# Optimization experiments

Measured on AMD Instinct MI355X. Metric: run time of the kernel, lower is better.

## Reference

```python
import jax, jax.numpy as jnp
import numpy as np

D_MODEL, D_FFN, N_LEVELS, N_HEADS, N_POINTS = 256, 1024, 4, 8, 4
B, LQ = 2, 8192
SHAPES = [(128, 128), (64, 64), (32, 32), (16, 16)]  # (H_l, W_l) per level
D_HEAD = D_MODEL // N_HEADS


def setup_inputs() -> dict:
    key = jax.random.key(0)
    ks = jax.random.split(key, 16)
    S = sum(h * w for h, w in SHAPES)

    def lin_w(k, fin, fout):
        s = 1.0 / np.sqrt(fin)
        return jax.random.uniform(k, (fin, fout), jnp.float32, -s, s)

    inp = {
        "tgt": jax.random.normal(ks[0], (B, LQ, D_MODEL), jnp.float32),
        "query_pos": jax.random.normal(ks[1], (B, LQ, D_MODEL), jnp.float32),
        "reference_points": jax.random.uniform(ks[2], (B, LQ, N_LEVELS, 2), jnp.float32),
        "src": jax.random.normal(ks[3], (B, S, D_MODEL), jnp.float32),
        "spatial_shapes": np.array(SHAPES, dtype=np.int64),
        "level_start_index": np.concatenate([[0], np.cumsum([h * w for h, w in SHAPES])[:-1]]).astype(np.int64),
        "W_value": lin_w(ks[4], D_MODEL, D_MODEL),
        "b_value": jnp.zeros((D_MODEL,), jnp.float32),
        "W_off": lin_w(ks[5], D_MODEL, N_HEADS * N_LEVELS * N_POINTS * 2),
        "b_off": 0.5 * jax.random.normal(ks[6], (N_HEADS * N_LEVELS * N_POINTS * 2,), jnp.float32),
        "W_attn": lin_w(ks[7], D_MODEL, N_HEADS * N_LEVELS * N_POINTS),
        "b_attn": jnp.zeros((N_HEADS * N_LEVELS * N_POINTS,), jnp.float32),
        "W_out": lin_w(ks[8], D_MODEL, D_MODEL),
        "b_out": jnp.zeros((D_MODEL,), jnp.float32),
        "ln1_g": jnp.ones((D_MODEL,), jnp.float32),
        "ln1_b": jnp.zeros((D_MODEL,), jnp.float32),
        "W1": lin_w(ks[9], D_MODEL, D_FFN),
        "b1": jnp.zeros((D_FFN,), jnp.float32),
        "W2": lin_w(ks[10], D_FFN, D_MODEL),
        "b2": jnp.zeros((D_MODEL,), jnp.float32),
        "ln3_g": jnp.ones((D_MODEL,), jnp.float32),
        "ln3_b": jnp.zeros((D_MODEL,), jnp.float32),
    }
    return inp


def _layer_norm(x, g, b, eps=1e-5):
    mu = jnp.mean(x, -1, keepdims=True)
    var = jnp.mean((x - mu) ** 2, -1, keepdims=True)
    return (x - mu) * jax.lax.rsqrt(var + eps) * g + b


def _ms_deform_attn(q, reference_points, src, shapes,
                    W_value, b_value, W_off, b_off, W_attn, b_attn, W_out, b_out):
    Bq, Lq, _ = q.shape
    value = (src @ W_value + b_value).reshape(Bq, -1, N_HEADS, D_HEAD)
    value = jnp.transpose(value, (0, 2, 1, 3))  # [B, H, S, Dh]
    off = (q @ W_off + b_off).reshape(Bq, Lq, N_HEADS, N_LEVELS, N_POINTS, 2)
    attn = jax.nn.softmax((q @ W_attn + b_attn).reshape(Bq, Lq, N_HEADS, N_LEVELS * N_POINTS), axis=-1)
    attn = attn.reshape(Bq, Lq, N_HEADS, N_LEVELS, N_POINTS)
    # offset normalizer is (W_l, H_l) per level
    normalizer = jnp.array([[w, h] for h, w in shapes], jnp.float32)
    loc = reference_points[:, :, None, :, None, :] + off / normalizer[None, None, None, :, None, :]

    out = jnp.zeros((Bq, Lq, N_HEADS, D_HEAD), jnp.float32)
    start = 0
    for l, (Hl, Wl) in enumerate(shapes):
        Nl = Hl * Wl
        v_l = value[:, :, start:start + Nl]  # [B, H, Nl, Dh]
        start += Nl
        loc_l = jnp.transpose(loc[:, :, :, l, :, :], (0, 2, 1, 3, 4))  # [B, H, Lq, P, 2]
        # grid_sample (align_corners=False, zero padding) pixel coords
        x = loc_l[..., 0] * Wl - 0.5
        y = loc_l[..., 1] * Hl - 0.5
        x0, y0 = jnp.floor(x), jnp.floor(y)
        wx, wy = x - x0, y - y0
        acc = jnp.zeros((Bq, N_HEADS, Lq, N_POINTS, D_HEAD), jnp.float32)
        for dx, dy, w in ((0, 0, (1 - wx) * (1 - wy)), (1, 0, wx * (1 - wy)),
                          (0, 1, (1 - wx) * wy), (1, 1, wx * wy)):
            xi, yi = x0 + dx, y0 + dy
            valid = (xi >= 0) & (xi < Wl) & (yi >= 0) & (yi < Hl)
            idx = (jnp.clip(yi, 0, Hl - 1) * Wl + jnp.clip(xi, 0, Wl - 1)).astype(jnp.int32)
            g = jnp.take_along_axis(v_l, idx.reshape(Bq, N_HEADS, -1, 1), axis=2)
            g = g.reshape(Bq, N_HEADS, Lq, N_POINTS, D_HEAD)
            acc = acc + jnp.where(valid[..., None], w[..., None] * g, 0.0)
        a = jnp.transpose(attn[:, :, :, l, :], (0, 2, 1, 3))  # [B, H, Lq, P]
        out = out + jnp.einsum('bhqp,bhqpd->bqhd', a, acc)
    return out.reshape(Bq, Lq, D_MODEL) @ W_out + b_out


def reference(tgt, query_pos, reference_points, src, spatial_shapes, level_start_index,
              W_value, b_value, W_off, b_off, W_attn, b_attn, W_out, b_out,
              ln1_g, ln1_b, W1, b1, W2, b2, ln3_g, ln3_b):
    shapes = [(int(h), int(w)) for h, w in np.asarray(spatial_shapes)]
    q = tgt + query_pos  # with_pos_embed
    tgt2 = _ms_deform_attn(q, reference_points, src, shapes,
                           W_value, b_value, W_off, b_off, W_attn, b_attn, W_out, b_out)
    x = _layer_norm(tgt + tgt2, ln1_g, ln1_b)  # dropout = identity (eval)
    ff = jax.nn.relu(x @ W1 + b1) @ W2 + b2
    return _layer_norm(x + ff, ln3_g, ln3_b)
```

## Files before the change

### kernel.cpp

```cpp
#include <hip/hip_runtime.h>
#include <hip/hip_bf16.h>
#include <hip/hip_fp16.h>
#include <math.h>

#define D_MODEL   256
#define D_FFN     1024
#define N_LEVELS  4
#define N_HEADS   8
#define N_POINTS  4
#define BATCH     2
#define LQ        8192
#define S_TOTAL   21760
#define M_Q       (BATCH*LQ)
#define M_V       (BATCH*S_TOTAL)
#define VT64      (M_V/64)

typedef __attribute__((ext_vector_type(8))) short bf16x8;
typedef __attribute__((ext_vector_type(4))) float floatx4;

struct alignas(8)  bh4 { __hip_bfloat16 a, b, c, d; };
struct alignas(16) bh8 { __hip_bfloat16 v[8]; };

__device__ __forceinline__ void gld_lds16(const void* g, void* l) {
    __builtin_amdgcn_global_load_lds(
        (const __attribute__((address_space(1))) void*)g,
        (__attribute__((address_space(3))) void*)l, 16, 0, 0);
}

__device__ __forceinline__ bh4 pack4(float4 a) {
    return { __float2bfloat16(a.x), __float2bfloat16(a.y),
             __float2bfloat16(a.z), __float2bfloat16(a.w) };
}

template<int K>
__device__ __forceinline__ void gemm_core64(const __hip_bfloat16* __restrict__ A,
                                            const __hip_bfloat16* __restrict__ Bt,
                                            int row0, int nb0, int lda, int ldb,
                                            short* As, short* Bs, floatx4 (&acc)[4])
{
    constexpr int NIT = K / 32;
    static_assert(NIT >= 2, "");
    const int tid  = threadIdx.x;
    const int w    = tid >> 6;
    const int lane = tid & 63;
    const int quad = lane >> 4;
    const int l15  = lane & 15;
    const size_t ldaB = (size_t)lda * 2, ldbB = (size_t)ldb * 2;

    const int o = w * 1024 + lane * 16;
    const char* gA = (const char*)A + (size_t)(row0 + (o >> 6)) * ldaB + (o & 63);
    const char* gB = (const char*)Bt + (size_t)(nb0 + (o >> 6)) * ldbB + (o & 63);
    const int lofs = w * 512;

    gld_lds16(gA,      As + lofs);
    gld_lds16(gB,      Bs + lofs);
    gld_lds16(gA + 64, As + 2048 + lofs);
    gld_lds16(gB + 64, Bs + 2048 + lofs);

    int oc = 0, on = 2048, of = 4096;
#pragma unroll
    for (int it = 0; it < NIT; ++it) {
        if (it + 1 < NIT) asm volatile("s_waitcnt vmcnt(2)" ::: "memory");
        else              asm volatile("s_waitcnt vmcnt(0)" ::: "memory");
        __builtin_amdgcn_s_barrier();
        __builtin_amdgcn_sched_barrier(0);
        if (it + 2 < NIT) {
            const size_t kb = (size_t)(it + 2) * 64;
            gld_lds16(gA + kb, As + of + lofs);
            gld_lds16(gB + kb, Bs + of + lofs);
        }
        const short* Ab = As + oc;
        const short* Bb = Bs + oc;
        bf16x8 af = *(const bf16x8*)&Ab[(w * 16 + l15) * 32 + quad * 8];
#pragma unroll
        for (int ni = 0; ni < 4; ni++) {
            bf16x8 bfr = *(const bf16x8*)&Bb[(ni * 16 + l15) * 32 + quad * 8];
            acc[ni] = __builtin_amdgcn_mfma_f32_16x16x32_bf16(af, bfr, acc[ni], 0, 0, 0);
        }
        int t = oc; oc = on; on = of; of = t;
    }
}

template<int K, bool ADD>
__device__ __forceinline__ void gemm_core_cvt64(const float* __restrict__ Af,
                                                const float* __restrict__ A2f,
                                                const __hip_bfloat16* __restrict__ Bt,
                                                int row0, int nb0, int lda, int ldb,
                                                short* As, short* Bs, floatx4 (&acc)[4])
{
    constexpr int NIT = K / 32;
    const int tid  = threadIdx.x;
    const int w    = tid >> 6;
    const int lane = tid & 63;
    const int quad = lane >> 4;
    const int l15  = lane & 15;

    const int o = w * 1024 + lane * 16;
    const char* gB = (const char*)Bt + (size_t)(nb0 + (o >> 6)) * ((size_t)ldb * 2) + (o & 63);
    const int lofs = w * 512;

    const int r0 = tid >> 3, k0 = (tid & 7) * 4;
    const float* gA0 = Af + (size_t)(row0 + r0) * lda + k0;
    const float* gA1 = gA0 + (size_t)32 * lda;
    const float* gB0 = ADD ? (A2f + (size_t)(row0 + r0) * lda + k0) : nullptr;
    const float* gB1 = ADD ? (gB0 + (size_t)32 * lda) : nullptr;
    const int aofs0 = r0 * 32 + k0, aofs1 = aofs0 + 1024;

    float4 f0, f1;
    auto loadA = [&](int kt) {
        f0 = *(const float4*)(gA0 + kt);
        f1 = *(const float4*)(gA1 + kt);
        if (ADD) {
            float4 a = *(const float4*)(gB0 + kt);
            float4 b = *(const float4*)(gB1 + kt);
            f0.x += a.x; f0.y += a.y; f0.z += a.z; f0.w += a.w;
            f1.x += b.x; f1.y += b.y; f1.z += b.z; f1.w += b.w;
        }
    };
    auto writeA = [&](short* buf) {
        *(bh4*)&buf[aofs0] = pack4(f0);
        *(bh4*)&buf[aofs1] = pack4(f1);
    };

    loadA(0);
    gld_lds16(gB, Bs + lofs);
    writeA(As);

#pragma unroll 8
    for (int it = 0; it < NIT; ++it) {
        __syncthreads();
        const int cb = it & 1;
        const bool more = (it + 1 < NIT);
        if (more) {
            loadA((it + 1) * 32);
            gld_lds16(gB + (size_t)(it + 1) * 64, Bs + (cb ^ 1) * 2048 + lofs);
        }
        const short* Ab = As + cb * 2048;
        const short* Bb = Bs + cb * 2048;
        bf16x8 af = *(const bf16x8*)&Ab[(w * 16 + l15) * 32 + quad * 8];
#pragma unroll
        for (int ni = 0; ni < 4; ni++) {
            bf16x8 bfr = *(const bf16x8*)&Bb[(ni * 16 + l15) * 32 + quad * 8];
            acc[ni] = __builtin_amdgcn_mfma_f32_16x16x32_bf16(af, bfr, acc[ni], 0, 0, 0);
        }
        if (more) writeA(As + (cb ^ 1) * 2048);
    }
}

template<int K, int EPI, int COLS>
__global__ __launch_bounds__(256)
void mfma_gemm64(const __hip_bfloat16* __restrict__ A,
                 const __hip_bfloat16* __restrict__ Bt,
                 const float* __restrict__ bias,
                 float* __restrict__ outf, __hip_bfloat16* __restrict__ outb,
                 int lda, int ldb, int ldOut)
{
    __shared__ alignas(16) short As[3 * 2048];
    __shared__ alignas(16) short Bs[3 * 2048];

    constexpr int BPG = 8 * COLS;
    const int g  = blockIdx.x / BPG;
    const int wq = blockIdx.x % BPG;
    const int row0 = (g * 8 + (wq & 7)) * 64;
    const int nb0  = (wq >> 3) * 64;

    const int tid = threadIdx.x, w = tid >> 6, lane = tid & 63;
    const int quad = lane >> 4, l15 = lane & 15;

    floatx4 acc[4];
#pragma unroll
    for (int ni = 0; ni < 4; ni++) acc[ni] = (floatx4){0.f, 0.f, 0.f, 0.f};

    gemm_core64<K>(A, Bt, row0, nb0, lda, ldb, As, Bs, acc);

    float bias_c[4];
#pragma unroll
    for (int ni = 0; ni < 4; ni++) bias_c[ni] = bias ? bias[nb0 + ni * 16 + l15] : 0.f;

#pragma unroll
    for (int r = 0; r < 4; r++) {
        int row = row0 + w * 16 + quad * 4 + r;
        size_t rb = (size_t)row * ldOut + nb0;
#pragma unroll
        for (int ni = 0; ni < 4; ni++) {
            float v = acc[ni][r] + bias_c[ni];
            if (EPI == 2)      outb[rb + ni * 16 + l15] = __float2bfloat16(fmaxf(v, 0.f));
            else if (EPI == 1) outb[rb + ni * 16 + l15] = __float2bfloat16(v);
            else               outf[rb + ni * 16 + l15] = v;
        }
    }
}

__global__ __launch_bounds__(256)
void mfma_gemm_vq(const float* __restrict__ src,
                  const __hip_bfloat16* __restrict__ Wvt,
                  const float* __restrict__ b_value,
                  __hip_bfloat16* __restrict__ valueb,
                  const float* __restrict__ tgt, const float* __restrict__ qpos,
                  const __hip_bfloat16* __restrict__ Woat,
                  const float* __restrict__ b_off, const float* __restrict__ b_attn,
                  float* __restrict__ offb, float* __restrict__ attnb)
{
    __shared__ alignas(16) short As[2 * 2048];
    __shared__ alignas(16) short Bs[2 * 2048];

    const int id = blockIdx.x;
    const int tid = threadIdx.x, w = tid >> 6, lane = tid & 63;
    const int quad = lane >> 4, l15 = lane & 15;

    floatx4 acc[4];
#pragma unroll
    for (int ni = 0; ni < 4; ni++) acc[ni] = (floatx4){0.f, 0.f, 0.f, 0.f};

    if (id < VT64 * 4) {
        const int g = id >> 5, wq = id & 31;
        const int row0 = (g * 8 + (wq & 7)) * 64;
        const int nb0  = (wq >> 3) * 64;
        gemm_core_cvt64<256, false>(src, nullptr, Wvt, row0, nb0, 256, 256, As, Bs, acc);
        float bias_c[4];
#pragma unroll
        for (int ni = 0; ni < 4; ni++) bias_c[ni] = b_value[nb0 + ni * 16 + l15];
#pragma unroll
        for (int r = 0; r < 4; r++) {
            int row = row0 + w * 16 + quad * 4 + r;
            size_t rb = (size_t)row * 256 + nb0;
#pragma unroll
            for (int ni = 0; ni < 4; ni++)
                valueb[rb + ni * 16 + l15] = __float2bfloat16(acc[ni][r] + bias_c[ni]);
        }
        return;
    }

    const int oid = id - VT64 * 4;
    const int g = oid / 48, wq = oid % 48;
    const int row0 = (g * 8 + (wq & 7)) * 64;
    const int c = wq >> 3;

    if (c < 4) {
        const int nb0 = c * 64;
        gemm_core_cvt64<256, true>(tgt, qpos, Woat, row0, nb0, 256, 256, As, Bs, acc);
        float bias_c[4];
#pragma unroll
        for (int ni = 0; ni < 4; ni++) bias_c[ni] = b_off[nb0 + ni * 16 + l15];
#pragma unroll
        for (int r = 0; r < 4; r++) {
            int row = row0 + w * 16 + quad * 4 + r;
            size_t rb = (size_t)row * 256 + nb0;
#pragma unroll
            for (int ni = 0; ni < 4; ni++)
                offb[rb + ni * 16 + l15] = acc[ni][r] + bias_c[ni];
        }
    } else {
        const int c0 = (c - 4) * 64;
        gemm_core_cvt64<256, true>(tgt, qpos, Woat, row0, 256 + c0, 256, 256, As, Bs, acc);
        float bias_c[4];
#pragma unroll
        for (int ni = 0; ni < 4; ni++) bias_c[ni] = b_attn[c0 + ni * 16 + l15];
#pragma unroll
        for (int r = 0; r < 4; r++) {
            int row = row0 + w * 16 + quad * 4 + r;
            size_t rb = (size_t)row * 128 + c0;
#pragma unroll
            for (int ni = 0; ni < 4; ni++) {
                float v = acc[ni][r] + bias_c[ni];
                float m = v;
#pragma unroll
                for (int msk = 1; msk <= 8; msk <<= 1) m = fmaxf(m, __shfl_xor(m, msk));
                float e = __expf(v - m);
                float ssum = e;
#pragma unroll
                for (int msk = 1; msk <= 8; msk <<= 1) ssum += __shfl_xor(ssum, msk);
                attnb[rb + ni * 16 + l15] = e / ssum;
            }
        }
    }
}

__global__ __launch_bounds__(512)
void ffn_fused(const __hip_bfloat16* __restrict__ xb,
               const __hip_bfloat16* __restrict__ W1t,
               const float* __restrict__ b1,
               const __hip_bfloat16* __restrict__ W2t,
               const float* __restrict__ b2,
               float* __restrict__ outf)
{
    __shared__ alignas(16) short xs[32 * 256];
    __shared__ alignas(16) short hs[32 * 1024];

    const int tid  = threadIdx.x;
    const int w    = tid >> 6;
    const int lane = tid & 63;
    const int quad = lane >> 4;
    const int l15  = lane & 15;
    const int row0 = blockIdx.x * 32;

    {
        const char* gx = (const char*)xb + (size_t)(row0 + (tid >> 5)) * 512 + (size_t)(tid & 31) * 16;
        char* dx = (char*)xs + (tid >> 6) * 1024;
        gld_lds16(gx, dx);
        gld_lds16(gx + 16 * 512, dx + 16 * 512);
    }
    __syncthreads();

    __hip_bfloat16* hsb = (__hip_bfloat16*)hs;

#pragma unroll
    for (int ci = 0; ci < 2; ci++) {
        const int c = w + ci * 8;
        const char* gW = (const char*)W1t + (size_t)(c * 64 + l15) * 512 + (size_t)quad * 16;

        floatx4 acc[2][4];
#pragma unroll
        for (int m = 0; m < 2; m++)
#pragma unroll
            for (int n = 0; n < 4; n++) acc[m][n] = (floatx4){0.f, 0.f, 0.f, 0.f};

        bf16x8 bcur[4], bnxt[4];
#pragma unroll
        for (int n = 0; n < 4; n++)
            bcur[n] = *(const bf16x8*)(gW + (size_t)n * 8192);

#pragma unroll
        for (int kk = 0; kk < 8; kk++) {
            if (kk + 1 < 8) {
#pragma unroll
                for (int n = 0; n < 4; n++)
                    bnxt[n] = *(const bf16x8*)(gW + (size_t)n * 8192 + (size_t)(kk + 1) * 64);
            }
            const int ac = (kk * 32 + quad * 8) ^ ((l15 & 7) << 3);
            bf16x8 a0 = *(const bf16x8*)&xs[(0 * 16 + l15) * 256 + ac];
            bf16x8 a1 = *(const bf16x8*)&xs[(1 * 16 + l15) * 256 + ac];
#pragma unroll
            for (int n = 0; n < 4; n++) {
                acc[0][n] = __builtin_amdgcn_mfma_f32_16x16x32_bf16(a0, bcur[n], acc[0][n], 0, 0, 0);
                acc[1][n] = __builtin_amdgcn_mfma_f32_16x16x32_bf16(a1, bcur[n], acc[1][n], 0, 0, 0);
            }
#pragma unroll
            for (int n = 0; n < 4; n++) bcur[n] = bnxt[n];
        }

#pragma unroll
        for (int n = 0; n < 4; n++) {
            const int hc = c * 64 + n * 16 + l15;
            const float bb = b1[hc];
#pragma unroll
            for (int m = 0; m < 2; m++)
#pragma unroll
                for (int r = 0; r < 4; r++) {
                    const int hr = m * 16 + quad * 4 + r;
                    hsb[hr * 1024 + (hc ^ ((hr & 7) << 3))] =
                        __float2bfloat16(fmaxf(acc[m][n][r] + bb, 0.f));
                }
        }
    }

    __syncthreads();

    const char* gW2 = (const char*)W2t + (size_t)(w * 32 + l15) * 2048 + (size_t)quad * 16;

    floatx4 acc2[2][2];
#pragma unroll
    for (int m = 0; m < 2; m++)
#pragma unroll
        for (int n = 0; n < 2; n++) acc2[m][n] = (floatx4){0.f, 0.f, 0.f, 0.f};

    bf16x8 c0[2], c1[2];
#pragma unroll
    for (int n = 0; n < 2; n++)
        c0[n] = *(const bf16x8*)(gW2 + (size_t)n * 32768);

#pragma unroll
    for (int kk = 0; kk < 32; kk++) {
        if (kk + 1 < 32) {
#pragma unroll
            for (int n = 0; n < 2; n++)
                c1[n] = *(const bf16x8*)(gW2 + (size_t)n * 32768 + (size_t)(kk + 1) * 64);
        }
        const int ac = (kk * 32 + quad * 8) ^ ((l15 & 7) << 3);
        bf16x8 a0 = *(const bf16x8*)&hs[(0 * 16 + l15) * 1024 + ac];
        bf16x8 a1 = *(const bf16x8*)&hs[(1 * 16 + l15) * 1024 + ac];
#pragma unroll
        for (int n = 0; n < 2; n++) {
            acc2[0][n] = __builtin_amdgcn_mfma_f32_16x16x32_bf16(a0, c0[n], acc2[0][n], 0, 0, 0);
            acc2[1][n] = __builtin_amdgcn_mfma_f32_16x16x32_bf16(a1, c0[n], acc2[1][n], 0, 0, 0);
        }
#pragma unroll
        for (int n = 0; n < 2; n++) c0[n] = c1[n];
    }

#pragma unroll
    for (int n = 0; n < 2; n++) {
        const int col = w * 32 + n * 16 + l15;
        const float bb = b2[col];
#pragma unroll
        for (int m = 0; m < 2; m++)
#pragma unroll
            for (int r = 0; r < 4; r++) {
                const int row = row0 + m * 16 + quad * 4 + r;
                outf[(size_t)row * 256 + col] = acc2[m][n][r] + bb;
            }
    }
}

template<bool B1>
__global__ __launch_bounds__(256)
void ln_kernel(const float* __restrict__ in1f, const __hip_bfloat16* __restrict__ in1b,
               const float* __restrict__ in2,
               const float* __restrict__ resid, const float* __restrict__ bias,
               const float* __restrict__ g, const float* __restrict__ b,
               float* __restrict__ outf, __hip_bfloat16* __restrict__ outb)
{
    const int row  = blockIdx.x * 4 + (threadIdx.x >> 6);
    const int lane = threadIdx.x & 63;
    const size_t rb = (size_t)row * 256 + lane * 4;

    float4 v = *(const float4*)(resid + rb);
    if (B1) {
        bh4 a = *(const bh4*)(in1b + rb);
        v.x += __bfloat162float(a.a); v.y += __bfloat162float(a.b);
        v.z += __bfloat162float(a.c); v.w += __bfloat162float(a.d);
    } else {
        float4 a = *(const float4*)(in1f + rb);
        v.x += a.x; v.y += a.y; v.z += a.z; v.w += a.w;
    }
    if (in2) {
        float4 c = *(const float4*)(in2 + rb);
        v.x += c.x; v.y += c.y; v.z += c.z; v.w += c.w;
    }
    if (bias) {
        float4 c = *(const float4*)(bias + lane * 4);
        v.x += c.x; v.y += c.y; v.z += c.z; v.w += c.w;
    }
    float s  = v.x + v.y + v.z + v.w;
    float sq = v.x * v.x + v.y * v.y + v.z * v.z + v.w * v.w;
#pragma unroll
    for (int msk = 1; msk <= 32; msk <<= 1) {
        s += __shfl_xor(s, msk); sq += __shfl_xor(sq, msk);
    }
    float mean = s * (1.f / 256.f);
    float var  = sq * (1.f / 256.f) - mean * mean;
    float rstd = rsqrtf(var + 1e-5f);
    float4 gg = *(const float4*)(g + lane * 4);
    float4 bb = *(const float4*)(b + lane * 4);
    float4 o;
    o.x = (v.x - mean) * rstd * gg.x + bb.x;
    o.y = (v.y - mean) * rstd * gg.y + bb.y;
    o.z = (v.z - mean) * rstd * gg.z + bb.z;
    o.w = (v.w - mean) * rstd * gg.w + bb.w;
    *(float4*)(outf + rb) = o;
    if (outb) {
        const int scol = (lane * 4) ^ ((row & 7) << 3);
        *(bh4*)(outb + (size_t)row * 256 + scol) =
            { __float2bfloat16(o.x), __float2bfloat16(o.y),
              __float2bfloat16(o.z), __float2bfloat16(o.w) };
    }
}

__global__ __launch_bounds__(256)
void prep_kernel(const float* w0, const float* w1, const float* w2,
                 const float* w3, const float* w4, const float* w5,
                 __hip_bfloat16* o0, __hip_bfloat16* o1, __hip_bfloat16* o2,
                 __hip_bfloat16* o3, __hip_bfloat16* o4, __hip_bfloat16* o5)
{
    int t = blockIdx.x;
    const float* s; __hip_bfloat16* dst; int Kd, Nd, tl;
    if      (t < 64)  { s = w0; dst = o0; Kd = 256;  Nd = 256;  tl = t; }
    else if (t < 128) { s = w1; dst = o1; Kd = 256;  Nd = 256;  tl = t - 64; }
    else if (t < 160) { s = w2; dst = o2; Kd = 256;  Nd = 128;  tl = t - 128; }
    else if (t < 224) { s = w3; dst = o3; Kd = 256;  Nd = 256;  tl = t - 160; }
    else if (t < 480) { s = w4; dst = o4; Kd = 256;  Nd = 1024; tl = t - 224; }
    else              { s = w5; dst = o5; Kd = 1024; Nd = 256;  tl = t - 480; }
    int ntn = Nd >> 5;
    int kt = tl / ntn, nt = tl - kt * ntn;
    __shared__ float T[32][33];
    int tx = threadIdx.x & 31, ty = threadIdx.x >> 5;
#pragma unroll
    for (int i = 0; i < 4; i++) {
        int k = kt * 32 + ty + i * 8;
        T[tx][ty + i * 8] = s[(size_t)k * Nd + nt * 32 + tx];
    }
    __syncthreads();
#pragma unroll
    for (int i = 0; i < 4; i++) {
        int n = nt * 32 + ty + i * 8;
        dst[(size_t)n * Kd + kt * 32 + tx] = __float2bfloat16(T[ty + i * 8][tx]);
    }
}

#define QB 8
__global__ __launch_bounds__(256, 4)
void sample_kernel(const float* __restrict__ refp, const float* __restrict__ offb,
                   const float* __restrict__ attn,
                   const __hip_bfloat16* __restrict__ value,
                   __hip_bfloat16* __restrict__ tgt2)
{
    __shared__ unsigned spk[64 * 65];

    const int q0  = blockIdx.x * QB;
    const int tid = threadIdx.x;

#pragma unroll
    for (int k = 0; k < 4; k++) {
        const int it = tid + k * 256;
        const int ql = it >> 7, h = (it >> 4) & 7, lp = it & 15;
        const int l = lp >> 2, p = lp & 3;
        const int q = q0 + ql, b = q >> 13;
        const int Wl = 128 >> l;
        const int LST = (l == 0) ? 0 : (l == 1) ? 16384 : (l == 2) ? 20480 : 21504;

        const float rx = refp[((size_t)q * N_LEVELS + l) * 2 + 0];
        const float ry = refp[((size_t)q * N_LEVELS + l) * 2 + 1];
        const float ox = offb[(size_t)q * 256 + h * 32 + l * 8 + p * 2 + 0];
        const float oy = offb[(size_t)q * 256 + h * 32 + l * 8 + p * 2 + 1];
        const float a  = attn[(size_t)q * 128 + h * 16 + lp];

        const float x = rx * Wl - 0.5f + ox;
        const float y = ry * Wl - 0.5f + oy;
        const float x0f = floorf(x), y0f = floorf(y);
        const float wx = x - x0f, wy = y - y0f;
        const int ix = (int)x0f, iy = (int)y0f;
        const int base = b * S_TOTAL + LST;
        const int g = ql * 8 + h;
        const float cw[4] = {(1.f - wx) * (1.f - wy) * a, wx * (1.f - wy) * a,
                             (1.f - wx) * wy * a,         wx * wy * a};
#pragma unroll
        for (int c = 0; c < 4; c++) {
            const int xi = ix + (c & 1), yi = iy + (c >> 1);
            const bool valid = ((unsigned)xi < (unsigned)Wl) && ((unsigned)yi < (unsigned)Wl);
            const unsigned pix = valid ? (unsigned)(base + yi * Wl + xi) : (unsigned)base;
            const __half hw = __float2half(valid ? cw[c] : 0.f);
            spk[(lp * 4 + c) * 65 + g] = (pix << 16) | (unsigned)__half_as_ushort(hw);
        }
    }
    __syncthreads();

    const int ql = tid >> 5, h = (tid >> 2) & 7, d4 = tid & 3;
    const int q = q0 + ql, g = ql * 8 + h;
    const int c0 = h * 32 + d4 * 8;
    const char* vb = (const char*)value + (size_t)c0 * 2;

    float ac[8] = {0.f, 0.f, 0.f, 0.f, 0.f, 0.f, 0.f, 0.f};
#pragma unroll
    for (int ch = 0; ch < 4; ch++) {
        unsigned us[16];
#pragma unroll
        for (int j = 0; j < 16; j++) us[j] = spk[(ch * 16 + j) * 65 + g];
        uint4 rv[16];
#pragma unroll
        for (int j = 0; j < 16; j++)
            rv[j] = *(const uint4*)(vb + ((size_t)(us[j] >> 16) << 9));
#pragma unroll
        for (int j = 0; j < 16; j++) {
            float wv = __half2float(__ushort_as_half((unsigned short)(us[j] & 0xffffu)));
            ac[0] += wv * __uint_as_float(rv[j].x << 16);
            ac[1] += wv * __uint_as_float(rv[j].x & 0xffff0000u);
            ac[2] += wv * __uint_as_float(rv[j].y << 16);
            ac[3] += wv * __uint_as_float(rv[j].y & 0xffff0000u);
            ac[4] += wv * __uint_as_float(rv[j].z << 16);
            ac[5] += wv * __uint_as_float(rv[j].z & 0xffff0000u);
            ac[6] += wv * __uint_as_float(rv[j].w << 16);
            ac[7] += wv * __uint_as_float(rv[j].w & 0xffff0000u);
        }
    }
    bh8 o;
#pragma unroll
    for (int i = 0; i < 8; i++) o.v[i] = __float2bfloat16(ac[i]);
    *(bh8*)(tgt2 + (size_t)q * 256 + c0) = o;
}

extern "C" void kernel_launch(void* const* d_in, const int* in_sizes, int n_in,
                              void* d_out, int out_size, void* d_ws, size_t ws_size,
                              hipStream_t stream) {
    const float* tgt     = (const float*)d_in[0];
    const float* qpos    = (const float*)d_in[1];
    const float* refp    = (const float*)d_in[2];
    const float* src     = (const float*)d_in[3];
    const float* W_value = (const float*)d_in[6];
    const float* b_value = (const float*)d_in[7];
    const float* W_off   = (const float*)d_in[8];
    const float* b_off   = (const float*)d_in[9];
    const float* W_attn  = (const float*)d_in[10];
    const float* b_attn  = (const float*)d_in[11];
    const float* W_out   = (const float*)d_in[12];
    const float* b_out   = (const float*)d_in[13];
    const float* ln1_g   = (const float*)d_in[14];
    const float* ln1_b   = (const float*)d_in[15];
    const float* W1      = (const float*)d_in[16];
    const float* b1      = (const float*)d_in[17];
    const float* W2      = (const float*)d_in[18];
    const float* b2      = (const float*)d_in[19];
    const float* ln3_g   = (const float*)d_in[20];
    const float* ln3_b   = (const float*)d_in[21];
    float* out = (float*)d_out;

    char* p = (char*)d_ws;
    auto nxt = [&](size_t b) { char* r = p; p += (b + 255) & ~(size_t)255; return r; };
    __hip_bfloat16* Wvt    = (__hip_bfloat16*)nxt((size_t)256 * 256 * 2);
    __hip_bfloat16* Woat   = (__hip_bfloat16*)nxt((size_t)384 * 256 * 2);
    __hip_bfloat16* Woutt  = (__hip_bfloat16*)nxt((size_t)256 * 256 * 2);
    __hip_bfloat16* W1t    = (__hip_bfloat16*)nxt((size_t)1024 * 256 * 2);
    __hip_bfloat16* W2t    = (__hip_bfloat16*)nxt((size_t)256 * 1024 * 2);
    __hip_bfloat16* valueb = (__hip_bfloat16*)nxt((size_t)M_V * 256 * 2);
    float*          offb   = (float*)nxt((size_t)M_Q * 256 * 4);
    float*          attnb  = (float*)nxt((size_t)M_Q * 128 * 4);
    __hip_bfloat16* tgt2b  = (__hip_bfloat16*)nxt((size_t)M_Q * 256 * 2);
    __hip_bfloat16* t2ob   = (__hip_bfloat16*)nxt((size_t)M_Q * 256 * 2);
    float*          x      = (float*)nxt((size_t)M_Q * 256 * 4);
    __hip_bfloat16* xb     = (__hip_bfloat16*)nxt((size_t)M_Q * 256 * 2);
    float* f2o = (float*)valueb;

    dim3 blk(256);

    prep_kernel<<<dim3(736), blk, 0, stream>>>(
        W_value, W_off, W_attn, W_out, W1, W2,
        Wvt, Woat, Woat + 256 * 256, Woutt, W1t, W2t);

    mfma_gemm_vq<<<dim3(VT64 * 4 + 256 / 8 * 48), blk, 0, stream>>>(
        src, Wvt, b_value, valueb, tgt, qpos, Woat, b_off, b_attn, offb, attnb);

    sample_kernel<<<dim3(M_Q / QB), blk, 0, stream>>>(refp, offb, attnb, valueb, tgt2b);

    mfma_gemm64<256, 1, 4><<<dim3(M_Q / 64 * 4), blk, 0, stream>>>(
        tgt2b, Woutt, b_out, nullptr, t2ob, 256, 256, 256);

    ln_kernel<true><<<dim3(M_Q / 4), blk, 0, stream>>>(
        nullptr, t2ob, nullptr, tgt, nullptr, ln1_g, ln1_b, x, xb);

    ffn_fused<<<dim3(M_Q / 32), dim3(512), 0, stream>>>(
        xb, W1t, b1, W2t, b2, f2o);

    ln_kernel<false><<<dim3(M_Q / 4), blk, 0, stream>>>(
        f2o, nullptr, nullptr, x, nullptr, ln3_g, ln3_b, out, nullptr);
}
```

Before: 316.4 us.

## Fuse final LayerNorm into FFN kernel and deepen weight prefetch pipelines

Folds the residual add and final LayerNorm into the fused FFN kernel's epilogue. The FFN output is staged through shared memory (padded rows), then normalized per row and written straight to the output, so the separate LN launch and its fp32 intermediate round-trip are gone. It also deepens the weight register prefetch to a 3-deep ring for W1 and a 4-deep ring for W2, with W2 prefetch started before the barrier. MFMA sections are wrapped in setprio, and launch bounds now request 4 blocks per CU. That adds register pressure and a hand-written barrier/waitcnt sequence. Variance uses E[x^2]-mean^2, which is slightly less numerically robust.

```diff
diff --git a/kernel.cpp b/kernel.cpp
--- a/kernel.cpp
+++ b/kernel.cpp
@@ -276,12 +276,14 @@
     }
 }
 
-__global__ __launch_bounds__(512)
+__global__ __launch_bounds__(512, 4)
 void ffn_fused(const __hip_bfloat16* __restrict__ xb,
                const __hip_bfloat16* __restrict__ W1t,
                const float* __restrict__ b1,
                const __hip_bfloat16* __restrict__ W2t,
                const float* __restrict__ b2,
+               const float* __restrict__ x,
+               const float* __restrict__ ln_g, const float* __restrict__ ln_b,
                float* __restrict__ outf)
 {
     __shared__ alignas(16) short xs[32 * 256];
@@ -315,28 +317,30 @@
 #pragma unroll
             for (int n = 0; n < 4; n++) acc[m][n] = (floatx4){0.f, 0.f, 0.f, 0.f};
 
-        bf16x8 bcur[4], bnxt[4];
-#pragma unroll
-        for (int n = 0; n < 4; n++)
-            bcur[n] = *(const bf16x8*)(gW + (size_t)n * 8192);
+        bf16x8 bq[3][4];
+#pragma unroll
+        for (int n = 0; n < 4; n++) {
+            bq[0][n] = *(const bf16x8*)(gW + (size_t)n * 8192);
+            bq[1][n] = *(const bf16x8*)(gW + (size_t)n * 8192 + 64);
+        }
 
 #pragma unroll
         for (int kk = 0; kk < 8; kk++) {
-            if (kk + 1 < 8) {
+            if (kk + 2 < 8) {
 #pragma unroll
                 for (int n = 0; n < 4; n++)
-                    bnxt[n] = *(const bf16x8*)(gW + (size_t)n * 8192 + (size_t)(kk + 1) * 64);
+                    bq[(kk + 2) % 3][n] = *(const bf16x8*)(gW + (size_t)n * 8192 + (size_t)(kk + 2) * 64);
             }
             const int ac = (kk * 32 + quad * 8) ^ ((l15 & 7) << 3);
-            bf16x8 a0 = *(const bf16x8*)&xs[(0 * 16 + l15) * 256 + ac];
-            bf16x8 a1 = *(const bf16x8*)&xs[(1 * 16 + l15) * 256 + ac];
+            bf16x8 a0 = *(const bf16x8*)&xs[l15 * 256 + ac];
+            bf16x8 a1 = *(const bf16x8*)&xs[(16 + l15) * 256 + ac];
+            __builtin_amdgcn_s_setprio(1);
 #pragma unroll
             for (int n = 0; n < 4; n++) {
-                acc[0][n] = __builtin_amdgcn_mfma_f32_16x16x32_bf16(a0, bcur[n], acc[0][n], 0, 0, 0);
-                acc[1][n] = __builtin_amdgcn_mfma_f32_16x16x32_bf16(a1, bcur[n], acc[1][n], 0, 0, 0);
+                acc[0][n] = __builtin_amdgcn_mfma_f32_16x16x32_bf16(a0, bq[kk % 3][n], acc[0][n], 0, 0, 0);
+                acc[1][n] = __builtin_amdgcn_mfma_f32_16x16x32_bf16(a1, bq[kk % 3][n], acc[1][n], 0, 0, 0);
             }
-#pragma unroll
-            for (int n = 0; n < 4; n++) bcur[n] = bnxt[n];
+            __builtin_amdgcn_s_setprio(0);
         }
 
 #pragma unroll
@@ -354,40 +358,45 @@
         }
     }
 
+    const char* gW2 = (const char*)W2t + (size_t)(w * 32 + l15) * 2048 + (size_t)quad * 16;
+    bf16x8 b2q[4][2];
+#pragma unroll
+    for (int j = 0; j < 3; j++)
+#pragma unroll
+        for (int n = 0; n < 2; n++)
+            b2q[j][n] = *(const bf16x8*)(gW2 + (size_t)n * 32768 + (size_t)j * 64);
+
+    asm volatile("s_waitcnt lgkmcnt(0)" ::: "memory");
+    __builtin_amdgcn_s_barrier();
+    __builtin_amdgcn_sched_barrier(0);
+
+    floatx4 acc2[2][2];
+#pragma unroll
+    for (int m = 0; m < 2; m++)
+#pragma unroll
+        for (int n = 0; n < 2; n++) acc2[m][n] = (floatx4){0.f, 0.f, 0.f, 0.f};
+
+#pragma unroll
+    for (int kk = 0; kk < 32; kk++) {
+        if (kk + 3 < 32) {
+#pragma unroll
+            for (int n = 0; n < 2; n++)
+                b2q[(kk + 3) & 3][n] = *(const bf16x8*)(gW2 + (size_t)n * 32768 + (size_t)(kk + 3) * 64);
+        }
+        const int ac = (kk * 32 + quad * 8) ^ ((l15 & 7) << 3);
+        bf16x8 a0 = *(const bf16x8*)&hs[l15 * 1024 + ac];
+        bf16x8 a1 = *(const bf16x8*)&hs[(16 + l15) * 1024 + ac];
+        __builtin_amdgcn_s_setprio(1);
+#pragma unroll
+        for (int n = 0; n < 2; n++) {
+            acc2[0][n] = __builtin_amdgcn_mfma_f32_16x16x32_bf16(a0, b2q[kk & 3][n], acc2[0][n], 0, 0, 0);
+            acc2[1][n] = __builtin_amdgcn_mfma_f32_16x16x32_bf16(a1, b2q[kk & 3][n], acc2[1][n], 0, 0, 0);
+        }
+        __builtin_amdgcn_s_setprio(0);
+    }
+
     __syncthreads();
-
-    const char* gW2 = (const char*)W2t + (size_t)(w * 32 + l15) * 2048 + (size_t)quad * 16;
-
-    floatx4 acc2[2][2];
-#pragma unroll
-    for (int m = 0; m < 2; m++)
-#pragma unroll
-        for (int n = 0; n < 2; n++) acc2[m][n] = (floatx4){0.f, 0.f, 0.f, 0.f};
-
-    bf16x8 c0[2], c1[2];
-#pragma unroll
-    for (int n = 0; n < 2; n++)
-        c0[n] = *(const bf16x8*)(gW2 + (size_t)n * 32768);
-
-#pragma unroll
-    for (int kk = 0; kk < 32; kk++) {
-        if (kk + 1 < 32) {
-#pragma unroll
-            for (int n = 0; n < 2; n++)
-                c1[n] = *(const bf16x8*)(gW2 + (size_t)n * 32768 + (size_t)(kk + 1) * 64);
-        }
-        const int ac = (kk * 32 + quad * 8) ^ ((l15 & 7) << 3);
-        bf16x8 a0 = *(const bf16x8*)&hs[(0 * 16 + l15) * 1024 + ac];
-        bf16x8 a1 = *(const bf16x8*)&hs[(1 * 16 + l15) * 1024 + ac];
-#pragma unroll
-        for (int n = 0; n < 2; n++) {
-            acc2[0][n] = __builtin_amdgcn_mfma_f32_16x16x32_bf16(a0, c0[n], acc2[0][n], 0, 0, 0);
-            acc2[1][n] = __builtin_amdgcn_mfma_f32_16x16x32_bf16(a1, c0[n], acc2[1][n], 0, 0, 0);
-        }
-#pragma unroll
-        for (int n = 0; n < 2; n++) c0[n] = c1[n];
-    }
-
+    float* osh = (float*)hs;
 #pragma unroll
     for (int n = 0; n < 2; n++) {
         const int col = w * 32 + n * 16 + l15;
@@ -396,9 +405,36 @@
         for (int m = 0; m < 2; m++)
 #pragma unroll
             for (int r = 0; r < 4; r++) {
-                const int row = row0 + m * 16 + quad * 4 + r;
-                outf[(size_t)row * 256 + col] = acc2[m][n][r] + bb;
+                const int row = m * 16 + quad * 4 + r;
+                osh[row * 260 + col] = acc2[m][n][r] + bb;
             }
+    }
+    __syncthreads();
+
+    float4 gg = *(const float4*)(ln_g + lane * 4);
+    float4 bbv = *(const float4*)(ln_b + lane * 4);
+#pragma unroll
+    for (int rr = 0; rr < 4; rr++) {
+        const int row = w * 4 + rr;
+        float4 f = *(const float4*)&osh[row * 260 + lane * 4];
+        float4 xr = *(const float4*)(x + (size_t)(row0 + row) * 256 + lane * 4);
+        float4 v;
+        v.x = f.x + xr.x; v.y = f.y + xr.y; v.z = f.z + xr.z; v.w = f.w + xr.w;
+        float s  = v.x + v.y + v.z + v.w;
+        float sq = v.x * v.x + v.y * v.y + v.z * v.z + v.w * v.w;
+#pragma unroll
+        for (int msk = 1; msk <= 32; msk <<= 1) {
+            s += __shfl_xor(s, msk); sq += __shfl_xor(sq, msk);
+        }
+        float mean = s * (1.f / 256.f);
+        float var  = sq * (1.f / 256.f) - mean * mean;
+        float rstd = rsqrtf(var + 1e-5f);
+        float4 o;
+        o.x = (v.x - mean) * rstd * gg.x + bbv.x;
+        o.y = (v.y - mean) * rstd * gg.y + bbv.y;
+        o.z = (v.z - mean) * rstd * gg.z + bbv.z;
+        o.w = (v.w - mean) * rstd * gg.w + bbv.w;
+        *(float4*)(outf + (size_t)(row0 + row) * 256 + lane * 4) = o;
     }
 }
 
@@ -607,7 +643,6 @@
     __hip_bfloat16* t2ob   = (__hip_bfloat16*)nxt((size_t)M_Q * 256 * 2);
     float*          x      = (float*)nxt((size_t)M_Q * 256 * 4);
     __hip_bfloat16* xb     = (__hip_bfloat16*)nxt((size_t)M_Q * 256 * 2);
-    float* f2o = (float*)valueb;
 
     dim3 blk(256);
 
@@ -627,8 +662,5 @@
         nullptr, t2ob, nullptr, tgt, nullptr, ln1_g, ln1_b, x, xb);
 
     ffn_fused<<<dim3(M_Q / 32), dim3(512), 0, stream>>>(
-        xb, W1t, b1, W2t, b2, f2o);
-
-    ln_kernel<false><<<dim3(M_Q / 4), blk, 0, stream>>>(
-        f2o, nullptr, nullptr, x, nullptr, ln3_g, ln3_b, out, nullptr);
-}
+        xb, W1t, b1, W2t, b2, x, ln3_g, ln3_b, out);
+}
```

Result: no change. 315.9 us (-0.2%).
